# Optimization experiments

Hardware: AMD Instinct MI355X
Metric: run time of the kernel (lower is better)

## Reference

```python
import jax, jax.numpy as jnp
import numpy as np

B, S, IN_DIM, HID = 8, 2048, 1024, 1024


def setup_inputs() -> dict:
    key = jax.random.key(0)
    k1, k2, k3, k4, k5 = jax.random.split(key, 5)
    vec = jax.random.normal(k1, (B, S, IN_DIM), dtype=jnp.float32)
    # nn.Linear-style init scale
    wq_w = jax.random.normal(k2, (HID, IN_DIM), dtype=jnp.float32) / np.sqrt(IN_DIM)
    wq_b = jax.random.normal(k3, (HID,), dtype=jnp.float32) * 0.02
    lin_w = jax.random.normal(k4, (1, HID), dtype=jnp.float32) / np.sqrt(HID)
    lin_b = jax.random.normal(k5, (1,), dtype=jnp.float32) * 0.02
    return {"vec": vec, "wq_w": wq_w, "wq_b": wq_b, "lin_w": lin_w, "lin_b": lin_b}


def reference(vec, wq_w, wq_b, lin_w, lin_b):
    # NOTE: the original forward applies self.wq to BOTH q and k (wk/nq/nk unused).
    q = jnp.einsum('bsi,hi->bsh', vec, wq_w) + wq_b          # [B,S,H]
    ret = jnp.einsum('bsx,bsy->bxy', q, q)                    # [B,H,H] bilinear
    ret = jax.nn.relu(ret)
    out = jnp.einsum('bxy,y->bx', ret, lin_w[0]) + lin_b[0]   # Linear(H,1) -> [B,H]
    return out
```

## Files before the change

kernel.cpp:

```cpp
#include <hip/hip_runtime.h>


typedef short     bf16x8 __attribute__((ext_vector_type(8)));
typedef unsigned short u16x8 __attribute__((ext_vector_type(8)));
typedef float     f32x4 __attribute__((ext_vector_type(4)));
typedef long long i64;

__device__ inline unsigned short f2bf(float f) {
  unsigned int u = __float_as_uint(f);
  u += 0x7fffu + ((u >> 16) & 1u);
  return (unsigned short)(u >> 16);
}

__device__ inline u16x8 pack8(float4 a, float4 b) {
  u16x8 r;
  r[0] = f2bf(a.x); r[1] = f2bf(a.y); r[2] = f2bf(a.z); r[3] = f2bf(a.w);
  r[4] = f2bf(b.x); r[5] = f2bf(b.y); r[6] = f2bf(b.z); r[7] = f2bf(b.w);
  return r;
}

__device__ inline unsigned char f2fp8(float v) {
  int pk = __builtin_amdgcn_cvt_pk_fp8_f32(v, v, 0, false);
  return (unsigned char)(pk & 0xff);
}

__device__ inline void async16(void* lds, const void* g) {
  __builtin_amdgcn_global_load_lds(
      (const __attribute__((address_space(1))) void*)g,
      (__attribute__((address_space(3))) void*)lds,
      16, 0, 0);
}

__global__ __launch_bounds__(256) void prep(
    const float* __restrict__ vec, unsigned short* __restrict__ vecbf,
    const float* __restrict__ wq,  unsigned short* __restrict__ wqbf,
    const float* __restrict__ lin_b, float* __restrict__ out)
{
  const int gid = blockIdx.x * 256 + threadIdx.x;
  if (blockIdx.x < 8192) {
    const float4* s = (const float4*)(vec + (size_t)gid * 8);
    float4 a = s[0], b = s[1];
    *(u16x8*)(vecbf + (size_t)gid * 8) = pack8(a, b);
    if (gid < 8192) out[gid] = lin_b[0];
  } else {
    const int i = gid - 8192 * 256;
    const float4* s = (const float4*)(wq + (size_t)i * 8);
    float4 a = s[0], b = s[1];
    *(u16x8*)(wqbf + (size_t)i * 8) = pack8(a, b);
  }
}

__global__ void init_out(float* __restrict__ out, const float* __restrict__ lin_b) {
  int i = blockIdx.x * 256 + threadIdx.x;
  if (i < 8192) out[i] = lin_b[0];
}

__global__ __launch_bounds__(256) void gemm_q(
    const unsigned short* __restrict__ A, const unsigned short* __restrict__ Bm,
    const float* __restrict__ bias, unsigned char* __restrict__ qT8)
{
  __shared__ unsigned short As[128 * 64];
  __shared__ unsigned short Bs[128 * 64];

  const int m0 = blockIdx.y * 128;
  const int n0 = blockIdx.x * 128;
  const int t    = threadIdx.x;
  const int lane = t & 63;
  const int wave = t >> 6;
  const int wm = (wave >> 1) * 64;
  const int wn = (wave & 1) * 64;
  const int quad = lane >> 4;
  const int lrow = lane & 15;

  const int srow = t >> 3;
  const int gcol = (((t & 7) ^ (srow & 7)) << 3);
  const unsigned short* gA = A  + (size_t)(m0 + srow) * 1024 + gcol;
  const unsigned short* gB = Bm + (size_t)(n0 + srow) * 1024 + gcol;

  f32x4 acc[4][4];
#pragma unroll
  for (int i = 0; i < 4; ++i)
#pragma unroll
    for (int j = 0; j < 4; ++j) acc[i][j] = (f32x4){0.f, 0.f, 0.f, 0.f};

  for (int k0 = 0; k0 < 1024; k0 += 64) {
#pragma unroll
    for (int p = 0; p < 4; ++p)
      async16(&As[p * 2048 + t * 8], gA + (size_t)p * 32 * 1024 + k0);
#pragma unroll
    for (int p = 0; p < 4; ++p)
      async16(&Bs[p * 2048 + t * 8], gB + (size_t)p * 32 * 1024 + k0);
    __syncthreads();

#pragma unroll
    for (int kk = 0; kk < 2; ++kk) {
      const int rc = (((kk * 4 + quad) ^ (lrow & 7)) << 3);
      bf16x8 af[4], bfr[4];
#pragma unroll
      for (int i = 0; i < 4; ++i)
        af[i] = *(const bf16x8*)&As[(wm + i * 16 + lrow) * 64 + rc];
#pragma unroll
      for (int j = 0; j < 4; ++j)
        bfr[j] = *(const bf16x8*)&Bs[(wn + j * 16 + lrow) * 64 + rc];
#pragma unroll
      for (int i = 0; i < 4; ++i)
#pragma unroll
        for (int j = 0; j < 4; ++j)
          acc[i][j] = __builtin_amdgcn_mfma_f32_16x16x32_bf16(af[i], bfr[j], acc[i][j], 0, 0, 0);
    }
    __syncthreads();
  }

#pragma unroll
  for (int i = 0; i < 4; ++i) {
    const int mb = m0 + wm + i * 16 + quad * 4;
#pragma unroll
    for (int r = 0; r < 4; ++r) {
      const float bv = bias[mb + r];
#pragma unroll
      for (int j = 0; j < 4; ++j) {
        const int n = n0 + wn + j * 16 + lrow;
        qT8[(size_t)(mb + r) * 16384 + n] = f2fp8(acc[i][j][r] + bv);
      }
    }
  }
}

__global__ __launch_bounds__(256) void gemm_q_fused(
    const float* __restrict__ Wq, const float* __restrict__ V,
    const float* __restrict__ bias, unsigned char* __restrict__ qT8)
{
  __shared__ unsigned short As[128 * 32];
  __shared__ unsigned short Bs[128 * 32];

  const int m0 = blockIdx.y * 128;
  const int n0 = blockIdx.x * 128;
  const int t    = threadIdx.x;
  const int lane = t & 63;
  const int wave = t >> 6;
  const int wm = (wave >> 1) * 64;
  const int wn = (wave & 1) * 64;
  const int quad = lane >> 4;
  const int lrow = lane & 15;

  const int sr = t >> 1;
  const int sc = (t & 1) << 4;
  const float* gA = Wq + (size_t)(m0 + sr) * 1024 + sc;
  const float* gB = V  + (size_t)(n0 + sr) * 1024 + sc;

  f32x4 acc[4][4];
#pragma unroll
  for (int i = 0; i < 4; ++i)
#pragma unroll
    for (int j = 0; j < 4; ++j) acc[i][j] = (f32x4){0.f, 0.f, 0.f, 0.f};

  for (int k0 = 0; k0 < 1024; k0 += 32) {
    const float4* a4 = (const float4*)(gA + k0);
    const float4* b4 = (const float4*)(gB + k0);
    float4 av0 = a4[0], av1 = a4[1], av2 = a4[2], av3 = a4[3];
    float4 bv0 = b4[0], bv1 = b4[1], bv2 = b4[2], bv3 = b4[3];
    *(u16x8*)&As[sr * 32 + sc]     = pack8(av0, av1);
    *(u16x8*)&As[sr * 32 + sc + 8] = pack8(av2, av3);
    *(u16x8*)&Bs[sr * 32 + sc]     = pack8(bv0, bv1);
    *(u16x8*)&Bs[sr * 32 + sc + 8] = pack8(bv2, bv3);
    __syncthreads();

    bf16x8 af[4], bfr[4];
#pragma unroll
    for (int i = 0; i < 4; ++i)
      af[i] = *(const bf16x8*)&As[(wm + i * 16 + lrow) * 32 + quad * 8];
#pragma unroll
    for (int j = 0; j < 4; ++j)
      bfr[j] = *(const bf16x8*)&Bs[(wn + j * 16 + lrow) * 32 + quad * 8];
#pragma unroll
    for (int i = 0; i < 4; ++i)
#pragma unroll
      for (int j = 0; j < 4; ++j)
        acc[i][j] = __builtin_amdgcn_mfma_f32_16x16x32_bf16(af[i], bfr[j], acc[i][j], 0, 0, 0);
    __syncthreads();
  }

#pragma unroll
  for (int i = 0; i < 4; ++i) {
    const int mb = m0 + wm + i * 16 + quad * 4;
#pragma unroll
    for (int r = 0; r < 4; ++r) {
      const float bv = bias[mb + r];
#pragma unroll
      for (int j = 0; j < 4; ++j) {
        const int n = n0 + wn + j * 16 + lrow;
        qT8[(size_t)(mb + r) * 16384 + n] = f2fp8(acc[i][j][r] + bv);
      }
    }
  }
}

__global__ __launch_bounds__(256) void syrk_half8(
    const unsigned char* __restrict__ qT8, const float* __restrict__ W,
    float* __restrict__ out)
{
  __shared__ unsigned char As[128 * 128];
  __shared__ unsigned char Bs[64 * 128];

  const int bb   = blockIdx.z;
  const int pair = blockIdx.x >> 1;
  const int yh   = blockIdx.x & 1;
  int tx = 0;
  while ((tx + 1) * (tx + 2) / 2 <= pair) ++tx;
  const int ty = pair - tx * (tx + 1) / 2;
  const int x0 = tx * 128;
  const int y0 = ty * 128 + yh * 64;
  const bool diag = (tx == ty);

  const int t    = threadIdx.x;
  const int lane = t & 63;
  const int wave = t >> 6;
  const int wm = (wave >> 1) * 64;
  const int wn = (wave & 1) * 32;
  const int quad = lane >> 4;
  const int lrow = lane & 15;

  const int srow = t >> 3;
  const int g16  = (t & 7) ^ (srow & 7);
  const size_t cb = (size_t)bb * 2048 + g16 * 16;
  const unsigned char* gA = qT8 + (size_t)(x0 + srow) * 16384 + cb;
  const unsigned char* gB = qT8 + (size_t)(y0 + srow) * 16384 + cb;

  f32x4 acc[4][2];
#pragma unroll
  for (int i = 0; i < 4; ++i)
#pragma unroll
    for (int j = 0; j < 2; ++j) acc[i][j] = (f32x4){0.f, 0.f, 0.f, 0.f};

  for (int k0 = 0; k0 < 2048; k0 += 128) {
#pragma unroll
    for (int p = 0; p < 4; ++p)
      async16(&As[p * 4096 + t * 16], gA + (size_t)p * 32 * 16384 + k0);
#pragma unroll
    for (int p = 0; p < 2; ++p)
      async16(&Bs[p * 4096 + t * 16], gB + (size_t)p * 32 * 16384 + k0);
    __syncthreads();

#pragma unroll
    for (int kk = 0; kk < 4; ++kk) {
      const int c = kk * 4 + quad;
      const int off = (((c >> 1) ^ (lrow & 7)) << 4) + (c & 1) * 8;
      i64 af[4], bfr[2];
#pragma unroll
      for (int i = 0; i < 4; ++i)
        af[i] = *(const i64*)&As[(wm + i * 16 + lrow) * 128 + off];
#pragma unroll
      for (int j = 0; j < 2; ++j)
        bfr[j] = *(const i64*)&Bs[(wn + j * 16 + lrow) * 128 + off];
#pragma unroll
      for (int i = 0; i < 4; ++i)
#pragma unroll
        for (int j = 0; j < 2; ++j)
          acc[i][j] = __builtin_amdgcn_mfma_f32_16x16x32_fp8_fp8(af[i], bfr[j], acc[i][j], 0, 0, 0);
    }
    __syncthreads();
  }

  float* ob = out + bb * 1024;

  float wv[2];
#pragma unroll
  for (int j = 0; j < 2; ++j) wv[j] = W[y0 + wn + j * 16 + lrow];

#pragma unroll
  for (int i = 0; i < 4; ++i) {
#pragma unroll
    for (int r = 0; r < 4; ++r) {
      float p = 0.f;
#pragma unroll
      for (int j = 0; j < 2; ++j) {
        float v = acc[i][j][r];
        v = v > 0.f ? v : 0.f;
        p += v * wv[j];
      }
#pragma unroll
      for (int off = 1; off < 16; off <<= 1) p += __shfl_xor(p, off, 64);
      if (lrow == 0)
        atomicAdd(&ob[x0 + wm + i * 16 + quad * 4 + r], p);
    }
  }

  if (!diag) {
    float wx[4][4];
#pragma unroll
    for (int i = 0; i < 4; ++i)
#pragma unroll
      for (int r = 0; r < 4; ++r)
        wx[i][r] = W[x0 + wm + i * 16 + quad * 4 + r];

#pragma unroll
    for (int j = 0; j < 2; ++j) {
      float pc = 0.f;
#pragma unroll
      for (int i = 0; i < 4; ++i)
#pragma unroll
        for (int r = 0; r < 4; ++r) {
          float v = acc[i][j][r];
          v = v > 0.f ? v : 0.f;
          pc += v * wx[i][r];
        }
      pc += __shfl_xor(pc, 16, 64);
      pc += __shfl_xor(pc, 32, 64);
      if (quad == 0)
        atomicAdd(&ob[y0 + wn + j * 16 + lrow], pc);
    }
  }
}

extern "C" void kernel_launch(void* const* d_in, const int* in_sizes, int n_in,
                              void* d_out, int out_size, void* d_ws, size_t ws_size,
                              hipStream_t stream) {
  const float* vec   = (const float*)d_in[0];
  const float* wq_w  = (const float*)d_in[1];
  const float* wq_b  = (const float*)d_in[2];
  const float* lin_w = (const float*)d_in[3];
  const float* lin_b = (const float*)d_in[4];
  float* out = (float*)d_out;

  unsigned char* qT8 = (unsigned char*)d_ws;
  const size_t need = (size_t)(16 + 32 + 2) * 1024 * 1024;

  if (ws_size >= need) {
    unsigned short* vecbf = (unsigned short*)((char*)d_ws + (size_t)16 * 1024 * 1024);
    unsigned short* wqbf  = vecbf + (size_t)16 * 1024 * 1024;
    prep<<<dim3(8192 + 512), dim3(256), 0, stream>>>(vec, vecbf, wq_w, wqbf, lin_b, out);
    gemm_q<<<dim3(128, 8), dim3(256), 0, stream>>>(wqbf, vecbf, wq_b, qT8);
  } else {
    init_out<<<dim3(32), dim3(256), 0, stream>>>(out, lin_b);
    gemm_q_fused<<<dim3(128, 8), dim3(256), 0, stream>>>(wq_w, vec, wq_b, qT8);
  }
  syrk_half8<<<dim3(72, 1, 8), dim3(256), 0, stream>>>(qT8, lin_w, out);
}
```

Before: 168.7 us.

## Rewrite Q GEMM as 256x256 tiled, double-buffered 8-wave pipelined kernel

Replaces the 128x128 single-buffered bf16 GEMM with a 256x256 tile kernel run by 512 threads. It double-buffers LDS and interleaves the async global-to-LDS loads of the next k-tile with MFMA work on quarter tiles, using explicit vmcnt waits, barriers and setprio. The aim is to hide global load latency and raise data reuse per tile. In exchange it uses 128KB of LDS per block and launches only 256 blocks, and the hand-written vmcnt ordering could be fragile.

```diff
diff --git a/kernel.cpp b/kernel.cpp
--- a/kernel.cpp
+++ b/kernel.cpp
@@ -55,75 +55,160 @@
   if (i < 8192) out[i] = lin_b[0];
 }
 
-__global__ __launch_bounds__(256) void gemm_q(
+__global__ __launch_bounds__(512, 2) void gemm_q8p(
     const unsigned short* __restrict__ A, const unsigned short* __restrict__ Bm,
     const float* __restrict__ bias, unsigned char* __restrict__ qT8)
 {
-  __shared__ unsigned short As[128 * 64];
-  __shared__ unsigned short Bs[128 * 64];
-
-  const int m0 = blockIdx.y * 128;
-  const int n0 = blockIdx.x * 128;
+  __shared__ unsigned short As[2][256 * 64];
+  __shared__ unsigned short Bs[2][256 * 64];
+
+  const int m0 = blockIdx.y * 256;
+  const int n0 = blockIdx.x * 256;
   const int t    = threadIdx.x;
   const int lane = t & 63;
   const int wave = t >> 6;
-  const int wm = (wave >> 1) * 64;
-  const int wn = (wave & 1) * 64;
+  const int wm2  = (wave >> 2) * 64;
+  const int wn2  = (wave & 3) * 32;
   const int quad = lane >> 4;
   const int lrow = lane & 15;
 
   const int srow = t >> 3;
-  const int gcol = (((t & 7) ^ (srow & 7)) << 3);
-  const unsigned short* gA = A  + (size_t)(m0 + srow) * 1024 + gcol;
-  const unsigned short* gB = Bm + (size_t)(n0 + srow) * 1024 + gcol;
-
-  f32x4 acc[4][4];
-#pragma unroll
-  for (int i = 0; i < 4; ++i)
-#pragma unroll
-    for (int j = 0; j < 4; ++j) acc[i][j] = (f32x4){0.f, 0.f, 0.f, 0.f};
-
-  for (int k0 = 0; k0 < 1024; k0 += 64) {
-#pragma unroll
-    for (int p = 0; p < 4; ++p)
-      async16(&As[p * 2048 + t * 8], gA + (size_t)p * 32 * 1024 + k0);
-#pragma unroll
-    for (int p = 0; p < 4; ++p)
-      async16(&Bs[p * 2048 + t * 8], gB + (size_t)p * 32 * 1024 + k0);
-    __syncthreads();
-
-#pragma unroll
-    for (int kk = 0; kk < 2; ++kk) {
-      const int rc = (((kk * 4 + quad) ^ (lrow & 7)) << 3);
-      bf16x8 af[4], bfr[4];
-#pragma unroll
-      for (int i = 0; i < 4; ++i)
-        af[i] = *(const bf16x8*)&As[(wm + i * 16 + lrow) * 64 + rc];
-#pragma unroll
-      for (int j = 0; j < 4; ++j)
-        bfr[j] = *(const bf16x8*)&Bs[(wn + j * 16 + lrow) * 64 + rc];
-#pragma unroll
-      for (int i = 0; i < 4; ++i)
-#pragma unroll
-        for (int j = 0; j < 4; ++j)
-          acc[i][j] = __builtin_amdgcn_mfma_f32_16x16x32_bf16(af[i], bfr[j], acc[i][j], 0, 0, 0);
-    }
-    __syncthreads();
-  }
-
-#pragma unroll
-  for (int i = 0; i < 4; ++i) {
-    const int mb = m0 + wm + i * 16 + quad * 4;
-#pragma unroll
-    for (int r = 0; r < 4; ++r) {
-      const float bv = bias[mb + r];
-#pragma unroll
-      for (int j = 0; j < 4; ++j) {
-        const int n = n0 + wn + j * 16 + lrow;
-        qT8[(size_t)(mb + r) * 16384 + n] = f2fp8(acc[i][j][r] + bv);
+  const int gch  = (t & 7) ^ (srow & 7);
+  const unsigned short* gA = A  + (size_t)(m0 + srow) * 1024 + gch * 8;
+  const unsigned short* gB = Bm + (size_t)(n0 + srow) * 1024 + gch * 8;
+
+#define VMCNT(N) asm volatile("s_waitcnt vmcnt(" #N ")" ::: "memory")
+#define BARR __builtin_amdgcn_s_barrier()
+
+#define STAGE_A(SLOT, H, KT) do { \
+  _Pragma("unroll") for (int p = 0; p < 2; ++p) \
+    async16(&As[SLOT][((H)*128 + p*64)*64 + t*8], \
+            gA + (size_t)((H)*128 + p*64)*1024 + (KT)*64); \
+} while (0)
+
+#define STAGE_B(SLOT, H, KT) do { \
+  _Pragma("unroll") for (int p = 0; p < 2; ++p) \
+    async16(&Bs[SLOT][((H)*128 + p*64)*64 + t*8], \
+            gB + (size_t)((H)*128 + p*64)*1024 + (KT)*64); \
+} while (0)
+
+#define LDA_HALF(S, MH) do { \
+  _Pragma("unroll") for (int f = 0; f < 4; ++f) \
+  _Pragma("unroll") for (int kk = 0; kk < 2; ++kk) \
+    a_[f][kk] = *(const bf16x8*)&As[S][((MH)*128 + wm2 + f*16 + lrow)*64 + \
+                                       (((kk*4 + quad) ^ (lrow & 7)) * 8)]; \
+} while (0)
+
+#define LDB_HALF(S, NH, BREG) do { \
+  _Pragma("unroll") for (int g = 0; g < 2; ++g) \
+  _Pragma("unroll") for (int kk = 0; kk < 2; ++kk) \
+    BREG[g][kk] = *(const bf16x8*)&Bs[S][((NH)*128 + wn2 + g*16 + lrow)*64 + \
+                                         (((kk*4 + quad) ^ (lrow & 7)) * 8)]; \
+} while (0)
+
+#define MFMAQ(MH, NH, BREG) do { \
+  __builtin_amdgcn_s_setprio(1); \
+  _Pragma("unroll") for (int kk = 0; kk < 2; ++kk) \
+  _Pragma("unroll") for (int f = 0; f < 4; ++f) \
+  _Pragma("unroll") for (int g = 0; g < 2; ++g) \
+    acc[MH][f][NH][g] = __builtin_amdgcn_mfma_f32_16x16x32_bf16( \
+        a_[f][kk], BREG[g][kk], acc[MH][f][NH][g], 0, 0, 0); \
+  __builtin_amdgcn_s_setprio(0); \
+} while (0)
+
+  f32x4 acc[2][4][2][2];
+#pragma unroll
+  for (int i = 0; i < 2; ++i)
+#pragma unroll
+    for (int f = 0; f < 4; ++f)
+#pragma unroll
+      for (int j = 0; j < 2; ++j)
+#pragma unroll
+        for (int g = 0; g < 2; ++g) acc[i][f][j][g] = (f32x4){0.f, 0.f, 0.f, 0.f};
+
+  bf16x8 a_[4][2], b0_[2][2], b1_[2][2];
+
+  STAGE_A(0, 0, 0);
+  STAGE_B(0, 0, 0);
+  STAGE_B(0, 1, 0);
+  STAGE_A(0, 1, 0);
+  VMCNT(4);
+  BARR;
+
+#pragma unroll 1
+  for (int kt = 0; kt < 15; ++kt) {
+    const int s  = kt & 1;
+    const int so = s ^ 1;
+
+    LDA_HALF(s, 0);
+    LDB_HALF(s, 0, b0_);
+    STAGE_A(so, 0, kt + 1);
+    VMCNT(4);
+    BARR;
+    MFMAQ(0, 0, b0_);
+    BARR;
+
+    LDB_HALF(s, 1, b1_);
+    STAGE_B(so, 0, kt + 1);
+    VMCNT(4);
+    BARR;
+    MFMAQ(0, 1, b1_);
+    BARR;
+
+    LDA_HALF(s, 1);
+    STAGE_B(so, 1, kt + 1);
+    VMCNT(4);
+    BARR;
+    MFMAQ(1, 0, b0_);
+    BARR;
+
+    STAGE_A(so, 1, kt + 1);
+    VMCNT(4);
+    BARR;
+    MFMAQ(1, 1, b1_);
+    BARR;
+  }
+
+  LDA_HALF(1, 0);
+  LDB_HALF(1, 0, b0_);
+  VMCNT(2);
+  BARR;
+  MFMAQ(0, 0, b0_);
+  BARR;
+
+  LDB_HALF(1, 1, b1_);
+  VMCNT(0);
+  BARR;
+  MFMAQ(0, 1, b1_);
+  BARR;
+
+  LDA_HALF(1, 1);
+  MFMAQ(1, 0, b0_);
+  MFMAQ(1, 1, b1_);
+
+#pragma unroll
+  for (int mh = 0; mh < 2; ++mh)
+#pragma unroll
+    for (int f = 0; f < 4; ++f)
+#pragma unroll
+      for (int r = 0; r < 4; ++r) {
+        const int m = m0 + mh * 128 + wm2 + f * 16 + quad * 4 + r;
+        const float bv = bias[m];
+        unsigned char* row = qT8 + (size_t)m * 16384 + n0;
+#pragma unroll
+        for (int nh = 0; nh < 2; ++nh)
+#pragma unroll
+          for (int g = 0; g < 2; ++g)
+            row[nh * 128 + wn2 + g * 16 + lrow] = f2fp8(acc[mh][f][nh][g][r] + bv);
       }
-    }
-  }
+
+#undef VMCNT
+#undef BARR
+#undef STAGE_A
+#undef STAGE_B
+#undef LDA_HALF
+#undef LDB_HALF
+#undef MFMAQ
 }
 
 __global__ __launch_bounds__(256) void gemm_q_fused(
@@ -329,7 +414,7 @@
     unsigned short* vecbf = (unsigned short*)((char*)d_ws + (size_t)16 * 1024 * 1024);
     unsigned short* wqbf  = vecbf + (size_t)16 * 1024 * 1024;
     prep<<<dim3(8192 + 512), dim3(256), 0, stream>>>(vec, vecbf, wq_w, wqbf, lin_b, out);
-    gemm_q<<<dim3(128, 8), dim3(256), 0, stream>>>(wqbf, vecbf, wq_b, qT8);
+    gemm_q8p<<<dim3(64, 4), dim3(512), 0, stream>>>(wqbf, vecbf, wq_b, qT8);
   } else {
     init_out<<<dim3(32), dim3(256), 0, stream>>>(out, lin_b);
     gemm_q_fused<<<dim3(128, 8), dim3(256), 0, stream>>>(wq_w, vec, wq_b, qT8);
```

After: 168.6 us. No clear change (-0.0%).
